# Optimization experiments

Hardware: AMD Instinct MI355X
Metric: run time of the kernel (lower is better)

## Reference

```python
import jax, jax.numpy as jnp
import numpy as np

B, X, Y, Z, C = 2, 96, 96, 64, 32
K_BG = K_FG = 8
LOG_PROB_SCALE = 200.0


def _make_gmm(key, K, C):
    k1, k2, k3 = jax.random.split(key, 3)
    # mixture weights divided by 2, as in the torch module
    w = jax.nn.softmax(jax.random.normal(k1, (K,))) / 2.0
    mu = jax.random.normal(k2, (K, C), dtype=jnp.float32)
    A = 0.1 * jax.random.normal(k3, (K, C, C), dtype=jnp.float32)
    d = 0.5 + jnp.abs(jnp.diagonal(A, axis1=-2, axis2=-1))  # positive diagonal
    L = jnp.tril(A, -1) + jax.vmap(jnp.diag)(d)             # valid lower Cholesky
    return w.astype(jnp.float32), mu, L


def setup_inputs() -> dict:
    key = jax.random.key(0)
    kf, kb, kg = jax.random.split(key, 3)
    feature_map = jax.random.normal(kf, (B, X, Y, Z, C), dtype=jnp.float32)
    w_bg, mu_bg, L_bg = _make_gmm(kb, K_BG, C)
    w_fg, mu_fg, L_fg = _make_gmm(kg, K_FG, C)
    return {
        "feature_map": feature_map,
        "weights_bg": w_bg, "means_bg": mu_bg, "chol_bg": L_bg,
        "weights_fg": w_fg, "means_fg": mu_fg, "chol_fg": L_fg,
    }


def reference(feature_map, weights_bg, means_bg, chol_bg,
              weights_fg, means_fg, chol_fg):
    Bv, Xv, Yv, Zv, Cv = feature_map.shape
    w = jnp.concatenate([weights_bg, weights_fg])      # [K]
    mu = jnp.concatenate([means_bg, means_fg])         # [K,C]
    L = jnp.concatenate([chol_bg, chol_fg])            # [K,C,C] lower tri

    eye = jnp.eye(Cv, dtype=L.dtype)
    Linv = jax.vmap(lambda l: jax.scipy.linalg.solve_triangular(l, eye, lower=True))(L)
    logdet = jnp.sum(jnp.log(jnp.diagonal(L, axis1=-2, axis2=-1)), axis=-1)  # [K]
    const = -0.5 * Cv * float(np.log(2.0 * np.pi))

    def body(dens, p):
        wk, muk, Lik, ldk = p
        # whitened residual y = L^{-1}(x - mu): [B,X,Y,Z,C]
        y = jnp.einsum('bxyzc,dc->bxyzd', feature_map - muk, Lik)
        logp = const - ldk - 0.5 * jnp.sum(y * y, axis=-1)  # MVN log_prob [B,X,Y,Z]
        return dens + wk * jnp.exp(logp / LOG_PROB_SCALE), None

    dens0 = jnp.zeros(feature_map.shape[:4], dtype=feature_map.dtype)
    dens, _ = jax.lax.scan(body, dens0, (w, mu, Linv, logdet))

    # torch loop runs frac in range(Z-1): last z-slice stays zero
    mask = (jnp.arange(Zv) < Zv - 1).astype(dens.dtype)
    dens = dens * mask  # broadcast over last axis
    return dens[:, None]  # [B,1,X,Y,Z]
```

## Files before the change

### kernel.cpp

```cpp
#include <hip/hip_runtime.h>
#include <hip/hip_bf16.h>
#include <cstring>

#define NVOX (2 * 96 * 96 * 64)
#define K_TOT 16
#define N_TILES (NVOX / 128)

typedef __attribute__((ext_vector_type(8)))  short short8;
typedef __attribute__((ext_vector_type(16))) float f32x16;
typedef __attribute__((ext_vector_type(2)))  float f32x2;

#define WS_UF 8192
#define WS_HW 8704
#define WS_FLOATS 8736

static __device__ __forceinline__ unsigned short f2b(float f) {
    __hip_bfloat16 h = __float2bfloat16(f);
    unsigned short u;
    __builtin_memcpy(&u, &h, 2);
    return u;
}

static __device__ __forceinline__ int pack2_bf16(float f0, float f1) {
    unsigned a, b;
    __builtin_memcpy(&a, &f0, 4);
    __builtin_memcpy(&b, &f1, 4);
    return (int)__builtin_amdgcn_perm(b + 0x8000u, a + 0x8000u, 0x07060302u);
}

static __device__ __forceinline__ short8 cvt8(float4 lo, float4 hi) {
    int p0 = pack2_bf16(lo.x, lo.y);
    int p1 = pack2_bf16(lo.z, lo.w);
    int p2 = pack2_bf16(hi.x, hi.y);
    int p3 = pack2_bf16(hi.z, hi.w);
    int v[4] = {p0, p1, p2, p3};
    short8 r;
    __builtin_memcpy(&r, v, 16);
    return r;
}

__global__ void gmm_prep_kernel(const float* __restrict__ wb, const float* __restrict__ mb,
                                const float* __restrict__ Lb, const float* __restrict__ wf,
                                const float* __restrict__ mf, const float* __restrict__ Lf,
                                float* __restrict__ ws) {
    int k   = blockIdx.x;
    int tid = threadIdx.x;

    __shared__ float Lsh[1024];
    __shared__ float Lish[1024];
    __shared__ float ush[32];

    const float* L  = (k < 8) ? (Lb + k * 1024) : (Lf + (k - 8) * 1024);
    const float* mu = (k < 8) ? (mb + k * 32)   : (mf + (k - 8) * 32);

    for (int i = tid; i < 1024; i += 64) Lsh[i] = L[i];
    __syncthreads();

    if (tid < 32) {
        int j = tid;
        float col[32];
#pragma unroll
        for (int i = 0; i < 32; ++i) {
            float s = (i == j) ? 1.0f : 0.0f;
#pragma unroll
            for (int m = 0; m < i; ++m) s = fmaf(-Lsh[i * 32 + m], col[m], s);
            float val = s / Lsh[i * 32 + i];
            col[i] = (i >= j) ? val : 0.0f;
        }
#pragma unroll
        for (int i = 0; i < 32; ++i) Lish[i * 32 + j] = col[i];
    }
    __syncthreads();
    if (tid < 32) {
        int d = tid;
        float s = 0.0f;
        for (int c = 0; c <= d; ++c) s = fmaf(Lish[d * 32 + c], mu[c], s);
        ush[d] = s;
    }
    __syncthreads();

    unsigned short* wsA = (unsigned short*)ws;
    int m  = tid & 31;
    int kq = tid >> 5;
#pragma unroll
    for (int hf = 0; hf < 2; ++hf) {
        unsigned short* dst = wsA + (size_t)(((k * 2 + hf) * 64 + tid) * 8);
#pragma unroll
        for (int j = 0; j < 8; ++j)
            dst[j] = f2b(Lish[m * 32 + hf * 16 + kq * 8 + j]);
    }
    if (tid < 32) {
        int h = tid >> 4, r = tid & 15;
        ws[WS_UF + k * 32 + tid] = -ush[(r & 3) + 8 * (r >> 2) + 4 * h];
    }
    if (tid == 0) {
        float ld = 0.0f;
        for (int i = 0; i < 32; ++i) ld += logf(Lsh[i * 32 + i]);
        const float cconst = -0.5f * 32.0f * 1.8378770664093453f;
        const float log2e  = 1.4426950408889634f;
        ws[WS_HW + k * 2]     = (cconst - ld) * (1.0f / 200.0f) * log2e;
        ws[WS_HW + k * 2 + 1] = (k < 8) ? wb[k] : wf[k - 8];
    }
}

__global__ __launch_bounds__(256, 4) void gmm_density_kernel(
        const float* __restrict__ fm, const float* __restrict__ ws,
        float* __restrict__ out) {
    __shared__ __align__(16) float smem[WS_FLOATS];
    {
        const float4* src = (const float4*)ws;
        float4* dst = (float4*)smem;
        for (int i = threadIdx.x; i < WS_FLOATS / 4; i += 256) dst[i] = src[i];
    }
    __syncthreads();
    const unsigned short* sWf = (const unsigned short*)smem;
    const float* sUf = smem + WS_UF;
    const float* sHW = smem + WS_HW;

    const int lane = threadIdx.x & 63;
    const int c    = lane & 31;
    const int h    = lane >> 5;
    const int tile = (blockIdx.x * 256 + (int)threadIdx.x) >> 6;
    size_t vbase = (size_t)tile * 128;

    const float SCALE = -0.0036067376022224085f;

    short8 Blo[4], Bhi[4];
#pragma unroll
    for (int g = 0; g < 4; ++g) {
        const float* xb = fm + (vbase + g * 32 + c) * 32 + h * 8;
        float4 a0 = *(const float4*)(xb + 0);
        float4 a1 = *(const float4*)(xb + 4);
        float4 b0 = *(const float4*)(xb + 16);
        float4 b1 = *(const float4*)(xb + 20);
        Blo[g] = cvt8(a0, a1);
        Bhi[g] = cvt8(b0, b1);
    }

    float dens[4] = {0.f, 0.f, 0.f, 0.f};
    for (int kc = 0; kc < K_TOT; ++kc) {
        short8 Alo = *(const short8*)(sWf + ((size_t)(kc * 2 + 0) * 64 + lane) * 8);
        short8 Ahi = *(const short8*)(sWf + ((size_t)(kc * 2 + 1) * 64 + lane) * 8);
        f32x16 Cu;
        {
            const float4* up = (const float4*)(sUf + kc * 32 + h * 16);
            float4 u0 = up[0], u1 = up[1], u2 = up[2], u3 = up[3];
            Cu[0]  = u0.x; Cu[1]  = u0.y; Cu[2]  = u0.z; Cu[3]  = u0.w;
            Cu[4]  = u1.x; Cu[5]  = u1.y; Cu[6]  = u1.z; Cu[7]  = u1.w;
            Cu[8]  = u2.x; Cu[9]  = u2.y; Cu[10] = u2.z; Cu[11] = u2.w;
            Cu[12] = u3.x; Cu[13] = u3.y; Cu[14] = u3.z; Cu[15] = u3.w;
        }
        float h2 = sHW[kc * 2], wk = sHW[kc * 2 + 1];
#pragma unroll
        for (int g = 0; g < 4; ++g) {
            f32x16 d = __builtin_amdgcn_mfma_f32_32x32x16_bf16(Alo, Blo[g], Cu, 0, 0, 0);
            d = __builtin_amdgcn_mfma_f32_32x32x16_bf16(Ahi, Bhi[g], d, 0, 0, 0);
            f32x2 acc0 = {0.f, 0.f}, acc1 = {0.f, 0.f};
#pragma unroll
            for (int r = 0; r < 4; ++r) {
                f32x2 y0, y1;
                y0[0] = d[4 * r + 0]; y0[1] = d[4 * r + 1];
                y1[0] = d[4 * r + 2]; y1[1] = d[4 * r + 3];
                asm("v_pk_fma_f32 %0, %1, %1, %0" : "+v"(acc0) : "v"(y0));
                asm("v_pk_fma_f32 %0, %1, %1, %0" : "+v"(acc1) : "v"(y1));
            }
            float p = (acc0[0] + acc0[1]) + (acc1[0] + acc1[1]);
            p += __shfl_xor(p, 32);
            dens[g] = fmaf(wk, __builtin_amdgcn_exp2f(fmaf(p, SCALE, h2)), dens[g]);
        }
    }

#pragma unroll
    for (int gg = 0; gg < 2; ++gg) {
        int g = h * 2 + gg;
        float val = dens[g];
        if (c == 31 && (g & 1)) val = 0.f;
        out[vbase + g * 32 + c] = val;
    }
}

extern "C" void kernel_launch(void* const* d_in, const int* in_sizes, int n_in,
                              void* d_out, int out_size, void* d_ws, size_t ws_size,
                              hipStream_t stream) {
    const float* fm = (const float*)d_in[0];
    const float* wb = (const float*)d_in[1];
    const float* mb = (const float*)d_in[2];
    const float* Lb = (const float*)d_in[3];
    const float* wf = (const float*)d_in[4];
    const float* mf = (const float*)d_in[5];
    const float* Lf = (const float*)d_in[6];
    float* out = (float*)d_out;
    float* ws  = (float*)d_ws;

    gmm_prep_kernel<<<K_TOT, 64, 0, stream>>>(wb, mb, Lb, wf, mf, Lf, ws);
    gmm_density_kernel<<<N_TILES / 4, 256, 0, stream>>>(fm, ws, out);
}
```

Before: 240.8 us.

## Process two voxel tiles per wave to amortize per-component LDS loads

Each wavefront now handles two 128-voxel tiles, one in each half of the volume, so the kernel launches half as many blocks. The per-component A-fragment, offset and weight loads from LDS, plus the per-block workspace copy into LDS, are shared across eight MFMA groups instead of four. The squared-sum reduction moves from inline v_pk_fma assembly to compiler vector arithmetic. This raises register pressure, since sixteen B fragments are held per lane, and halves the wave count, which may reduce latency hiding for the memory-bound feature-map load.

```diff
diff --git a/kernel.cpp b/kernel.cpp
--- a/kernel.cpp
+++ b/kernel.cpp
@@ -5,6 +5,7 @@
 #define NVOX (2 * 96 * 96 * 64)
 #define K_TOT 16
 #define N_TILES (NVOX / 128)
+#define N_WAVES (N_TILES / 2)
 
 typedef __attribute__((ext_vector_type(8)))  short short8;
 typedef __attribute__((ext_vector_type(16))) float f32x16;
@@ -120,62 +121,63 @@
     const int lane = threadIdx.x & 63;
     const int c    = lane & 31;
     const int h    = lane >> 5;
-    const int tile = (blockIdx.x * 256 + (int)threadIdx.x) >> 6;
-    size_t vbase = (size_t)tile * 128;
+    const int gwave = (blockIdx.x * 256 + (int)threadIdx.x) >> 6;
+    size_t vbase0 = (size_t)gwave * 128;
+    size_t vbase1 = (size_t)(gwave + N_WAVES) * 128;
 
     const float SCALE = -0.0036067376022224085f;
 
-    short8 Blo[4], Bhi[4];
+    short8 B[8][2];
 #pragma unroll
-    for (int g = 0; g < 4; ++g) {
-        const float* xb = fm + (vbase + g * 32 + c) * 32 + h * 8;
-        float4 a0 = *(const float4*)(xb + 0);
-        float4 a1 = *(const float4*)(xb + 4);
-        float4 b0 = *(const float4*)(xb + 16);
-        float4 b1 = *(const float4*)(xb + 20);
-        Blo[g] = cvt8(a0, a1);
-        Bhi[g] = cvt8(b0, b1);
+    for (int t = 0; t < 2; ++t) {
+        size_t vb = t ? vbase1 : vbase0;
+#pragma unroll
+        for (int g = 0; g < 4; ++g) {
+            const float* xb = fm + (vb + g * 32 + c) * 32 + h * 8;
+            float4 a0 = *(const float4*)(xb + 0);
+            float4 a1 = *(const float4*)(xb + 4);
+            float4 b0 = *(const float4*)(xb + 16);
+            float4 b1 = *(const float4*)(xb + 20);
+            B[t * 4 + g][0] = cvt8(a0, a1);
+            B[t * 4 + g][1] = cvt8(b0, b1);
+        }
     }
 
-    float dens[4] = {0.f, 0.f, 0.f, 0.f};
+    float dens[8] = {0.f, 0.f, 0.f, 0.f, 0.f, 0.f, 0.f, 0.f};
     for (int kc = 0; kc < K_TOT; ++kc) {
         short8 Alo = *(const short8*)(sWf + ((size_t)(kc * 2 + 0) * 64 + lane) * 8);
         short8 Ahi = *(const short8*)(sWf + ((size_t)(kc * 2 + 1) * 64 + lane) * 8);
-        f32x16 Cu;
-        {
-            const float4* up = (const float4*)(sUf + kc * 32 + h * 16);
-            float4 u0 = up[0], u1 = up[1], u2 = up[2], u3 = up[3];
-            Cu[0]  = u0.x; Cu[1]  = u0.y; Cu[2]  = u0.z; Cu[3]  = u0.w;
-            Cu[4]  = u1.x; Cu[5]  = u1.y; Cu[6]  = u1.z; Cu[7]  = u1.w;
-            Cu[8]  = u2.x; Cu[9]  = u2.y; Cu[10] = u2.z; Cu[11] = u2.w;
-            Cu[12] = u3.x; Cu[13] = u3.y; Cu[14] = u3.z; Cu[15] = u3.w;
-        }
+        f32x16 Cu = *(const f32x16*)(sUf + kc * 32 + h * 16);
         float h2 = sHW[kc * 2], wk = sHW[kc * 2 + 1];
 #pragma unroll
-        for (int g = 0; g < 4; ++g) {
-            f32x16 d = __builtin_amdgcn_mfma_f32_32x32x16_bf16(Alo, Blo[g], Cu, 0, 0, 0);
-            d = __builtin_amdgcn_mfma_f32_32x32x16_bf16(Ahi, Bhi[g], d, 0, 0, 0);
-            f32x2 acc0 = {0.f, 0.f}, acc1 = {0.f, 0.f};
+        for (int g = 0; g < 8; ++g) {
+            f32x16 d = __builtin_amdgcn_mfma_f32_32x32x16_bf16(Alo, B[g][0], Cu, 0, 0, 0);
+            d = __builtin_amdgcn_mfma_f32_32x32x16_bf16(Ahi, B[g][1], d, 0, 0, 0);
+            const f32x2* dp = (const f32x2*)&d;
+            f32x2 acc0 = dp[0] * dp[0];
+            f32x2 acc1 = dp[1] * dp[1];
 #pragma unroll
-            for (int r = 0; r < 4; ++r) {
-                f32x2 y0, y1;
-                y0[0] = d[4 * r + 0]; y0[1] = d[4 * r + 1];
-                y1[0] = d[4 * r + 2]; y1[1] = d[4 * r + 3];
-                asm("v_pk_fma_f32 %0, %1, %1, %0" : "+v"(acc0) : "v"(y0));
-                asm("v_pk_fma_f32 %0, %1, %1, %0" : "+v"(acc1) : "v"(y1));
+            for (int r = 1; r < 4; ++r) {
+                acc0 += dp[2 * r + 0] * dp[2 * r + 0];
+                acc1 += dp[2 * r + 1] * dp[2 * r + 1];
             }
-            float p = (acc0[0] + acc0[1]) + (acc1[0] + acc1[1]);
+            f32x2 accs = acc0 + acc1;
+            float p = accs[0] + accs[1];
             p += __shfl_xor(p, 32);
             dens[g] = fmaf(wk, __builtin_amdgcn_exp2f(fmaf(p, SCALE, h2)), dens[g]);
         }
     }
 
 #pragma unroll
-    for (int gg = 0; gg < 2; ++gg) {
-        int g = h * 2 + gg;
-        float val = dens[g];
-        if (c == 31 && (g & 1)) val = 0.f;
-        out[vbase + g * 32 + c] = val;
+    for (int t = 0; t < 2; ++t) {
+        size_t vb = t ? vbase1 : vbase0;
+#pragma unroll
+        for (int gg = 0; gg < 2; ++gg) {
+            int g = h * 2 + gg;
+            float val = dens[t * 4 + g];
+            if (c == 31 && (g & 1)) val = 0.f;
+            out[vb + g * 32 + c] = val;
+        }
     }
 }
 
@@ -193,5 +195,5 @@
     float* ws  = (float*)d_ws;
 
     gmm_prep_kernel<<<K_TOT, 64, 0, stream>>>(wb, mb, Lb, wf, mf, Lf, ws);
-    gmm_density_kernel<<<N_TILES / 4, 256, 0, stream>>>(fm, ws, out);
+    gmm_density_kernel<<<N_WAVES / 4, 256, 0, stream>>>(fm, ws, out);
 }
```

Measured after the change: 247.4 us. 2.7% more time.
